# Performance work log

Hardware: AMD Instinct MI355X
Metric: run time of the kernel (lower is better)

The kernel has to match this reference:

```python
import jax, jax.numpy as jnp
import numpy as np

B, L, M, H = 16, 1024, 1024, 128
NEG = -1e30


def setup_inputs() -> dict:
    key = jax.random.key(0)
    ks = jax.random.split(key, 8)
    return {
        "text": jax.random.normal(ks[0], (B, L, H), dtype=jnp.float32),
        "modality": jax.random.normal(ks[1], (B, M, H), dtype=jnp.float32),
        "text_mask": jax.random.randint(ks[2], (B, L), 0, 2, dtype=jnp.int32),
        "modality_mask": jax.random.randint(ks[3], (B, M), 0, 2, dtype=jnp.int32),
        # learned parameters (xavier-uniform style scale)
        "text_weight": jax.random.normal(ks[4], (H, 1), dtype=jnp.float32) * 0.1,
        "modality_weight": jax.random.normal(ks[5], (H, 1), dtype=jnp.float32) * 0.1,
        "text_modality_weight": jax.random.normal(ks[6], (1, 1, H), dtype=jnp.float32) * 0.1,
        "bias": jnp.zeros((1,), dtype=jnp.float32),
    }


def reference(text, modality, text_mask, modality_mask,
              text_weight, modality_weight, text_modality_weight, bias):
    # similarity matrix s: (B, L, M)   (eval mode: dropout is identity)
    s0 = jnp.matmul(text, text_weight)                      # (B, L, 1)
    s1 = jnp.swapaxes(jnp.matmul(modality, modality_weight), 1, 2)  # (B, 1, M)
    s2 = jnp.einsum('blh,bmh->blm', text * text_modality_weight, modality)
    s = s0 + s1 + s2 + bias                                 # (B, L, M)

    mmask = modality_mask[:, None, :].astype(jnp.float32)   # (B, 1, M)
    tmask = text_mask[:, :, None].astype(jnp.float32)       # (B, L, 1)
    p1 = jax.nn.softmax(mmask * s + (1.0 - mmask) * NEG, axis=2)  # text->modality
    p2 = jax.nn.softmax(tmask * s + (1.0 - tmask) * NEG, axis=1)  # modality->text

    a = jnp.matmul(p1, modality)                            # (B, L, H)
    b = jnp.matmul(jnp.matmul(p1, jnp.swapaxes(p2, 1, 2)), text)  # (B, L, H)
    return jnp.concatenate([text, a, text * a, text * b], axis=2)  # (B, L, 8H)
```

## Files before the change

kernel.cpp:

```cpp
#include <hip/hip_runtime.h>

#define B_ 16
#define L_ 1024
#define M_ 1024
#define H_ 128

typedef unsigned short u16;
typedef unsigned int u32;
typedef __bf16 bf16x8 __attribute__((ext_vector_type(8)));
typedef float f32x4 __attribute__((ext_vector_type(4)));

__device__ __forceinline__ u16 f2bf(float x){
  u32 u = __float_as_uint(x);
  u = (u + 0x7fffu + ((u >> 16) & 1u)) >> 16;
  return (u16)u;
}

__global__ __launch_bounds__(256) void zero_f32(float4* __restrict__ p, int n4)
{
  int i = blockIdx.x * 256 + threadIdx.x;
  int stride = gridDim.x * 256;
  for (; i < n4; i += stride) p[i] = make_float4(0.f, 0.f, 0.f, 0.f);
}

__global__ __launch_bounds__(256) void prep2(
    const float* __restrict__ text, const float* __restrict__ modality,
    const int* __restrict__ tmask, const int* __restrict__ mmask,
    const float* __restrict__ tw, const float* __restrict__ mw,
    const float* __restrict__ tmw,
    u16* __restrict__ textw_bf, u16* __restrict__ mod_bf,
    u16* __restrict__ textT_bf, u16* __restrict__ modT_bf,
    float* __restrict__ t0, float* __restrict__ s1m)
{
  int g = blockIdx.x;
  int sel = g >> 8;
  int b = (g >> 4) & 15;
  int r0 = (g & 15) * 64;
  const float* src = (sel ? modality : text) + ((size_t)b * 1024 + r0) * H_;
  const int* msk = (sel ? mmask : tmask) + b * 1024 + r0;
  const float* dotw = sel ? mw : tw;
  u16* rowout = (sel ? mod_bf : textw_bf) + ((size_t)b * 1024 + r0) * H_;
  u16* trout = (sel ? modT_bf : textT_bf) + (size_t)b * H_ * 1024 + r0;
  float* dotout = (sel ? s1m : t0) + b * 1024 + r0;

  __shared__ u16 tile[128][72];
  int tid = threadIdx.x;
  int rgrp = tid >> 5;
  int lane32 = tid & 31;
  int h0 = lane32 * 4;
  float4 w4 = *(const float4*)&dotw[h0];
  float4 mv = sel ? make_float4(1.f, 1.f, 1.f, 1.f) : *(const float4*)&tmw[h0];
  float dpart[8];
  #pragma unroll
  for (int p = 0; p < 8; p++) {
    int row = rgrp + p * 8;
    float4 x = *(const float4*)&src[(size_t)row * H_ + h0];
    dpart[p] = x.x * w4.x + x.y * w4.y + x.z * w4.z + x.w * w4.w;
    uint2 pk;
    pk.x = (u32)f2bf(x.x * mv.x) | ((u32)f2bf(x.y * mv.y) << 16);
    pk.y = (u32)f2bf(x.z * mv.z) | ((u32)f2bf(x.w * mv.w) << 16);
    *(uint2*)&rowout[(size_t)row * H_ + h0] = pk;
    int mk = msk[row];
    tile[h0 + 0][row] = mk ? f2bf(x.x) : (u16)0;
    tile[h0 + 1][row] = mk ? f2bf(x.y) : (u16)0;
    tile[h0 + 2][row] = mk ? f2bf(x.z) : (u16)0;
    tile[h0 + 3][row] = mk ? f2bf(x.w) : (u16)0;
  }
  #pragma unroll
  for (int p = 0; p < 8; p++) {
    float d = dpart[p];
    #pragma unroll
    for (int off = 1; off < 32; off <<= 1) d += __shfl_xor(d, off);
    if (lane32 == 0) dotout[rgrp + p * 8] = d;
  }
  __syncthreads();
  int lcol = (tid & 7) * 8;
  #pragma unroll
  for (int p = 0; p < 4; p++) {
    int h = (tid >> 3) + p * 32;
    uint4 v = *(const uint4*)&tile[h][lcol];
    *(uint4*)&trout[(size_t)h * 1024 + lcol] = v;
  }
}

__global__ __launch_bounds__(256) void gemm_exp(
    const u16* __restrict__ A, const u16* __restrict__ Bm,
    const float* __restrict__ t0, const float* __restrict__ s1m,
    const float* __restrict__ bias, const int* __restrict__ tmask,
    const int* __restrict__ mmask, float* __restrict__ rowsum,
    float* __restrict__ colsum, u16* __restrict__ ET)
{
  int f = blockIdx.x;
  int orig = (f & 7) * 256 + (f >> 3);
  int b = orig >> 7;
  int a0 = (orig & 15) * 64, b0 = ((orig >> 4) & 7) * 128;
  int tid = threadIdx.x, lane = tid & 63, wid = tid >> 6;
  int wr = wid >> 1, wc = wid & 1;
  int c = lane & 15, q = lane >> 4;
  __shared__ __align__(16) char smem[24576];
  const u16* Ab = A + (size_t)(b * L_ + a0) * H_;
  const u16* Bb = Bm + (size_t)(b * M_ + b0) * H_;
  f32x4 acc[2][4];
  #pragma unroll
  for (int i = 0; i < 2; i++)
    #pragma unroll
    for (int j = 0; j < 4; j++) acc[i][j] = (f32x4){0.f, 0.f, 0.f, 0.f};
  for (int kt = 0; kt < 2; kt++) {
    __syncthreads();
    #pragma unroll
    for (int i = 0; i < 2; i++) {
      int cc = tid + 256 * i;
      int row = cc >> 3, col8 = cc & 7;
      uint4 v = *(const uint4*)(Ab + (size_t)row * H_ + kt * 64 + col8 * 8);
      *(uint4*)(smem + row * 128 + ((col8 * 16) ^ ((row & 7) << 4))) = v;
    }
    #pragma unroll
    for (int i = 0; i < 4; i++) {
      int cc = tid + 256 * i;
      int row = cc >> 3, col8 = cc & 7;
      uint4 v = *(const uint4*)(Bb + (size_t)row * H_ + kt * 64 + col8 * 8);
      *(uint4*)(smem + 8192 + row * 128 + ((col8 * 16) ^ ((row & 7) << 4))) = v;
    }
    __syncthreads();
    #pragma unroll
    for (int kk = 0; kk < 2; kk++) {
      int kbyte = kk * 64 + (q << 4);
      bf16x8 af[2], bfr[4];
      #pragma unroll
      for (int i = 0; i < 2; i++) {
        int ra = wr * 32 + i * 16 + c;
        af[i] = *(const bf16x8*)(smem + ra * 128 + (kbyte ^ ((ra & 7) << 4)));
      }
      #pragma unroll
      for (int j = 0; j < 4; j++) {
        int rb = wc * 64 + j * 16 + c;
        bfr[j] = *(const bf16x8*)(smem + 8192 + rb * 128 + (kbyte ^ ((rb & 7) << 4)));
      }
      #pragma unroll
      for (int i = 0; i < 2; i++)
        #pragma unroll
        for (int j = 0; j < 4; j++)
          acc[i][j] = __builtin_amdgcn_mfma_f32_16x16x32_bf16(af[i], bfr[j], acc[i][j], 0, 0, 0);
    }
  }
  float biasv = bias[0];
  float t0v[2][4];
  int tmv[2][4];
  #pragma unroll
  for (int i = 0; i < 2; i++)
    #pragma unroll
    for (int r = 0; r < 4; r++) {
      int ar = a0 + wr * 32 + i * 16 + q * 4 + r;
      t0v[i][r] = t0[b * L_ + ar];
      tmv[i][r] = tmask[b * L_ + ar];
    }
  float s1v[4];
  int mmv[4];
  #pragma unroll
  for (int j = 0; j < 4; j++) {
    int gcol = b0 + wc * 64 + j * 16 + c;
    s1v[j] = s1m[b * M_ + gcol];
    mmv[j] = mmask[b * M_ + gcol];
  }
  float ev[2][4][4];
  #pragma unroll
  for (int i = 0; i < 2; i++)
    #pragma unroll
    for (int j = 0; j < 4; j++)
      #pragma unroll
      for (int r = 0; r < 4; r++)
        ev[i][j][r] = __expf(acc[i][j][r] + t0v[i][r] + s1v[j] + biasv);
  #pragma unroll
  for (int i = 0; i < 2; i++)
    #pragma unroll
    for (int r = 0; r < 4; r++) {
      float prs = 0.f;
      #pragma unroll
      for (int j = 0; j < 4; j++) prs += mmv[j] ? ev[i][j][r] : 0.f;
      #pragma unroll
      for (int off = 1; off < 16; off <<= 1) prs += __shfl_xor(prs, off);
      if (c == 0) {
        int ar = a0 + wr * 32 + i * 16 + q * 4 + r;
        atomicAdd(&rowsum[b * L_ + ar], prs);
      }
    }
  #pragma unroll
  for (int j = 0; j < 4; j++) {
    float pcs = 0.f;
    #pragma unroll
    for (int i = 0; i < 2; i++)
      #pragma unroll
      for (int r = 0; r < 4; r++) pcs += tmv[i][r] ? ev[i][j][r] : 0.f;
    pcs += __shfl_xor(pcs, 16);
    pcs += __shfl_xor(pcs, 32);
    if (q == 0) {
      int gcol = b0 + wc * 64 + j * 16 + c;
      atomicAdd(&colsum[b * M_ + gcol], pcs);
    }
  }
  __syncthreads();
  u16* et = (u16*)smem;
  #pragma unroll
  for (int i = 0; i < 2; i++)
    #pragma unroll
    for (int j = 0; j < 4; j++) {
      int gcolL = wc * 64 + j * 16 + c;
      int arL = wr * 32 + i * 16 + q * 4;
      u32 lo = (u32)f2bf(ev[i][j][0]) | ((u32)f2bf(ev[i][j][1]) << 16);
      u32 hi = (u32)f2bf(ev[i][j][2]) | ((u32)f2bf(ev[i][j][3]) << 16);
      uint2 pk; pk.x = lo; pk.y = hi;
      *(uint2*)&et[gcolL * 72 + arL] = pk;
    }
  __syncthreads();
  #pragma unroll
  for (int it = 0; it < 4; it++) {
    int mrow = (tid >> 3) + it * 32;
    int l8 = tid & 7;
    uint4 v = *(const uint4*)&et[mrow * 72 + l8 * 8];
    *(uint4*)&ET[((size_t)(b * M_ + b0 + mrow)) * L_ + a0 + l8 * 8] = v;
  }
}

__global__ __launch_bounds__(512) void gemm_ct(
    const u16* __restrict__ A, const u16* __restrict__ ET,
    float* __restrict__ c_f32)
{
  int f = blockIdx.x;
  int orig = (f & 7) * 64 + (f >> 3);
  int b = orig >> 5;
  int x = orig & 3, y = (orig >> 2) & 7;
  int ia = x & 1, ks = x >> 1;
  int a0 = ia * 64, b0 = y * 128;
  int tid = threadIdx.x, lane = tid & 63, wid = tid >> 6;
  int wr = wid >> 2, wc = wid & 3;
  int c = lane & 15, q = lane >> 4;
  __shared__ __align__(16) char smem[24576];
  const u16* Ab = A + (size_t)(b * H_ + a0) * L_;
  const u16* Bb = ET + (size_t)(b * M_ + b0) * L_;
  f32x4 acc[2][2];
  #pragma unroll
  for (int i = 0; i < 2; i++)
    #pragma unroll
    for (int j = 0; j < 2; j++) acc[i][j] = (f32x4){0.f, 0.f, 0.f, 0.f};
  for (int kt = ks * 8; kt < ks * 8 + 8; kt++) {
    __syncthreads();
    {
      int row = tid >> 3, col8 = tid & 7;
      uint4 v = *(const uint4*)(Ab + (size_t)row * L_ + kt * 64 + col8 * 8);
      *(uint4*)(smem + row * 128 + ((col8 * 16) ^ ((row & 7) << 4))) = v;
    }
    #pragma unroll
    for (int i = 0; i < 2; i++) {
      int cc = tid + 512 * i;
      int row = cc >> 3, col8 = cc & 7;
      uint4 v = *(const uint4*)(Bb + (size_t)row * L_ + kt * 64 + col8 * 8);
      *(uint4*)(smem + 8192 + row * 128 + ((col8 * 16) ^ ((row & 7) << 4))) = v;
    }
    __syncthreads();
    #pragma unroll
    for (int kk = 0; kk < 2; kk++) {
      int kbyte = kk * 64 + (q << 4);
      bf16x8 af[2], bfr[2];
      #pragma unroll
      for (int i = 0; i < 2; i++) {
        int ra = wr * 32 + i * 16 + c;
        af[i] = *(const bf16x8*)(smem + ra * 128 + (kbyte ^ ((ra & 7) << 4)));
      }
      #pragma unroll
      for (int j = 0; j < 2; j++) {
        int rb = wc * 32 + j * 16 + c;
        bfr[j] = *(const bf16x8*)(smem + 8192 + rb * 128 + (kbyte ^ ((rb & 7) << 4)));
      }
      #pragma unroll
      for (int i = 0; i < 2; i++)
        #pragma unroll
        for (int j = 0; j < 2; j++)
          acc[i][j] = __builtin_amdgcn_mfma_f32_16x16x32_bf16(af[i], bfr[j], acc[i][j], 0, 0, 0);
    }
  }
  #pragma unroll
  for (int i = 0; i < 2; i++)
    #pragma unroll
    for (int j = 0; j < 2; j++) {
      int arow0 = a0 + wr * 32 + i * 16 + q * 4;
      int gcol = b0 + wc * 32 + j * 16 + c;
      #pragma unroll
      for (int r = 0; r < 4; r++)
        atomicAdd(&c_f32[((size_t)(b * H_ + arow0 + r)) * M_ + gcol], acc[i][j][r]);
    }
}

__global__ __launch_bounds__(512) void gemm_ab(
    const u16* __restrict__ ET, const u16* __restrict__ B1,
    const float* __restrict__ c_f32, const float* __restrict__ colsum,
    const int* __restrict__ mmask, const float* __restrict__ rowsum,
    const float* __restrict__ text, float* __restrict__ out)
{
  int f = blockIdx.x;
  int orig = (f & 7) * 32 + (f >> 3);
  int b = orig >> 4;
  int a0 = (orig & 15) * 64;
  int tid = threadIdx.x, lane = tid & 63, wid = tid >> 6;
  int wr = wid >> 2, wc = wid & 3;
  int c = lane & 15, q = lane >> 4;
  __shared__ __align__(16) u16 At[64 * 76];
  __shared__ __align__(16) char Bs[2][16384];
  __shared__ float invcm[1024];
  const u16* ETb = ET + (size_t)b * M_ * L_;
  const u16* B1b = B1 + (size_t)b * H_ * M_;
  const float* cfb = c_f32 + (size_t)b * H_ * M_;
  for (int i = tid; i < 1024; i += 512)
    invcm[i] = mmask[b * M_ + i] ? 1.0f / fmaxf(colsum[b * M_ + i], 1e-30f) : 0.f;
  f32x4 acc_a[2][2], acc_b[2][2];
  #pragma unroll
  for (int i = 0; i < 2; i++)
    #pragma unroll
    for (int j = 0; j < 2; j++) {
      acc_a[i][j] = (f32x4){0.f, 0.f, 0.f, 0.f};
      acc_b[i][j] = (f32x4){0.f, 0.f, 0.f, 0.f};
    }
  for (int kt = 0; kt < 16; kt++) {
    __syncthreads();
    {
      int mloc = tid >> 3, l8 = tid & 7;
      uint4 v = *(const uint4*)&ETb[((size_t)(kt * 64 + mloc)) * L_ + a0 + l8 * 8];
      u16* rp = At + mloc * 76 + l8 * 8;
      uint2 p0; p0.x = v.x; p0.y = v.y;
      uint2 p1; p1.x = v.z; p1.y = v.w;
      *(uint2*)rp = p0;
      *(uint2*)(rp + 4) = p1;
    }
    #pragma unroll
    for (int i = 0; i < 2; i++) {
      int cc = tid + 512 * i;
      int row = cc >> 3, col8 = cc & 7;
      uint4 v1 = *(const uint4*)(B1b + (size_t)row * M_ + kt * 64 + col8 * 8);
      *(uint4*)(Bs[0] + row * 128 + ((col8 * 16) ^ ((row & 7) << 4))) = v1;
      int mbase = kt * 64 + col8 * 8;
      float4 xa = *(const float4*)&cfb[(size_t)row * M_ + mbase];
      float4 xb = *(const float4*)&cfb[(size_t)row * M_ + mbase + 4];
      float4 ia4 = *(const float4*)&invcm[mbase];
      float4 ib4 = *(const float4*)&invcm[mbase + 4];
      uint4 v2;
      v2.x = (u32)f2bf(xa.x * ia4.x) | ((u32)f2bf(xa.y * ia4.y) << 16);
      v2.y = (u32)f2bf(xa.z * ia4.z) | ((u32)f2bf(xa.w * ia4.w) << 16);
      v2.z = (u32)f2bf(xb.x * ib4.x) | ((u32)f2bf(xb.y * ib4.y) << 16);
      v2.w = (u32)f2bf(xb.z * ib4.z) | ((u32)f2bf(xb.w * ib4.w) << 16);
      *(uint4*)(Bs[1] + row * 128 + ((col8 * 16) ^ ((row & 7) << 4))) = v2;
    }
    __syncthreads();
    #pragma unroll
    for (int kk = 0; kk < 2; kk++) {
      int kbyte = kk * 64 + (q << 4);
      bf16x8 af[2], b1f[2], b2f[2];
      #pragma unroll
      for (int i = 0; i < 2; i++) {
        int lidx = wr * 32 + i * 16 + c;
        int mbase = kk * 32 + q * 8;
        union { unsigned short s[8]; bf16x8 v; } ua;
        #pragma unroll
        for (int e = 0; e < 8; e++) ua.s[e] = At[(mbase + e) * 76 + lidx];
        af[i] = ua.v;
      }
      #pragma unroll
      for (int j = 0; j < 2; j++) {
        int rb = wc * 32 + j * 16 + c;
        b1f[j] = *(const bf16x8*)(Bs[0] + rb * 128 + (kbyte ^ ((rb & 7) << 4)));
        b2f[j] = *(const bf16x8*)(Bs[1] + rb * 128 + (kbyte ^ ((rb & 7) << 4)));
      }
      #pragma unroll
      for (int i = 0; i < 2; i++)
        #pragma unroll
        for (int j = 0; j < 2; j++) {
          acc_a[i][j] = __builtin_amdgcn_mfma_f32_16x16x32_bf16(af[i], b1f[j], acc_a[i][j], 0, 0, 0);
          acc_b[i][j] = __builtin_amdgcn_mfma_f32_16x16x32_bf16(af[i], b2f[j], acc_b[i][j], 0, 0, 0);
        }
    }
  }
  float irs[2][4];
  #pragma unroll
  for (int i = 0; i < 2; i++)
    #pragma unroll
    for (int r = 0; r < 4; r++) {
      int ar = a0 + wr * 32 + i * 16 + q * 4 + r;
      irs[i][r] = 1.0f / fmaxf(rowsum[b * L_ + ar], 1e-30f);
    }
  #pragma unroll
  for (int i = 0; i < 2; i++)
    #pragma unroll
    for (int j = 0; j < 2; j++) {
      int gcol = wc * 32 + j * 16 + c;
      #pragma unroll
      for (int r = 0; r < 4; r++) {
        int ar = a0 + wr * 32 + i * 16 + q * 4 + r;
        float av = acc_a[i][j][r] * irs[i][r];
        float bv = acc_b[i][j][r] * irs[i][r];
        float tv = text[((size_t)(b * L_ + ar)) * H_ + gcol];
        size_t base = ((size_t)(b * L_ + ar)) * 512 + gcol;
        out[base] = tv;
        out[base + 128] = av;
        out[base + 256] = tv * av;
        out[base + 384] = tv * bv;
      }
    }
}

extern "C" void kernel_launch(void* const* d_in, const int* in_sizes, int n_in,
                              void* d_out, int out_size, void* d_ws, size_t ws_size,
                              hipStream_t stream) {
  const float* text = (const float*)d_in[0];
  const float* modality = (const float*)d_in[1];
  const int* text_mask = (const int*)d_in[2];
  const int* modality_mask = (const int*)d_in[3];
  const float* text_weight = (const float*)d_in[4];
  const float* modality_weight = (const float*)d_in[5];
  const float* tmw = (const float*)d_in[6];
  const float* bias = (const float*)d_in[7];
  float* out = (float*)d_out;
  (void)in_sizes; (void)n_in; (void)out_size; (void)ws_size;

  char* ws = (char*)d_ws;
  size_t off = 0;
  auto alloc = [&](size_t bytes) { void* p = ws + off; off += (bytes + 255) & ~(size_t)255; return p; };
  u16*   ET       = (u16*)  alloc((size_t)B_ * M_ * L_ * 2);
  u16*   textw_bf = (u16*)  alloc((size_t)B_ * L_ * H_ * 2);
  u16*   mod_bf   = (u16*)  alloc((size_t)B_ * M_ * H_ * 2);
  u16*   textT_bf = (u16*)  alloc((size_t)B_ * H_ * L_ * 2);
  u16*   mod_bfT  = (u16*)  alloc((size_t)B_ * H_ * M_ * 2);
  float* t0       = (float*)alloc((size_t)B_ * L_ * 4);
  float* s1m      = (float*)alloc((size_t)B_ * M_ * 4);
  float* rowsum   = (float*)alloc((size_t)B_ * L_ * 4);
  float* colsum   = (float*)alloc((size_t)B_ * M_ * 4);
  float* c_f32    = (float*)alloc((size_t)B_ * H_ * M_ * 4);

  int n4 = (B_ * (L_ + M_) + B_ * H_ * M_) / 4;
  zero_f32<<<2048, 256, 0, stream>>>((float4*)rowsum, n4);
  prep2<<<512, 256, 0, stream>>>(text, modality, text_mask, modality_mask,
      text_weight, modality_weight, tmw,
      textw_bf, mod_bf, textT_bf, mod_bfT, t0, s1m);
  gemm_exp<<<2048, 256, 0, stream>>>(textw_bf, mod_bf, t0, s1m, bias,
      text_mask, modality_mask, rowsum, colsum, ET);
  gemm_ct<<<512, 512, 0, stream>>>(textT_bf, ET, c_f32);
  gemm_ab<<<256, 512, 0, stream>>>(ET, mod_bfT, c_f32, colsum, modality_mask,
      rowsum, text, out);
}
```

Before: 181.2 us.

## Double the gemm_ab block to 1024 threads and prefetch next K tile into registers

gemm_ab now runs with 1024 threads (16 waves), each wave owning a 32x16 output tile instead of 32x32. It also stages global loads for the next K tile into registers while MFMAs run on the current shared-memory tile. Both aim to hide global memory latency in a grid of only 256 blocks that cannot fill the GPU. The cost is more register pressure per thread under the larger launch bound, an extra barrier per iteration, and less MFMA work per wave.

```diff
diff --git a/kernel.cpp b/kernel.cpp
--- a/kernel.cpp
+++ b/kernel.cpp
@@ -290,7 +290,7 @@
     }
 }
 
-__global__ __launch_bounds__(512) void gemm_ab(
+__global__ __launch_bounds__(1024) void gemm_ab(
     const u16* __restrict__ ET, const u16* __restrict__ B1,
     const float* __restrict__ c_f32, const float* __restrict__ colsum,
     const int* __restrict__ mmask, const float* __restrict__ rowsum,
@@ -301,7 +301,7 @@
   int b = orig >> 4;
   int a0 = (orig & 15) * 64;
   int tid = threadIdx.x, lane = tid & 63, wid = tid >> 6;
-  int wr = wid >> 2, wc = wid & 3;
+  int wr = wid >> 3, wc = wid & 7;
   int c = lane & 15, q = lane >> 4;
   __shared__ __align__(16) u16 At[64 * 76];
   __shared__ __align__(16) char Bs[2][16384];
@@ -309,50 +309,53 @@
   const u16* ETb = ET + (size_t)b * M_ * L_;
   const u16* B1b = B1 + (size_t)b * H_ * M_;
   const float* cfb = c_f32 + (size_t)b * H_ * M_;
-  for (int i = tid; i < 1024; i += 512)
-    invcm[i] = mmask[b * M_ + i] ? 1.0f / fmaxf(colsum[b * M_ + i], 1e-30f) : 0.f;
-  f32x4 acc_a[2][2], acc_b[2][2];
-  #pragma unroll
-  for (int i = 0; i < 2; i++)
-    #pragma unroll
-    for (int j = 0; j < 2; j++) {
-      acc_a[i][j] = (f32x4){0.f, 0.f, 0.f, 0.f};
-      acc_b[i][j] = (f32x4){0.f, 0.f, 0.f, 0.f};
-    }
+  invcm[tid] = mmask[b * M_ + tid] ? 1.0f / fmaxf(colsum[b * M_ + tid], 1e-30f) : 0.f;
+
+  int sArow = tid >> 4, sAcol = (tid & 15) * 4;
+  int sBrow = tid >> 3, sBcol8 = tid & 7;
+
+  f32x4 acc_a[2], acc_b[2];
+  #pragma unroll
+  for (int i = 0; i < 2; i++) {
+    acc_a[i] = (f32x4){0.f, 0.f, 0.f, 0.f};
+    acc_b[i] = (f32x4){0.f, 0.f, 0.f, 0.f};
+  }
+
+  uint2 rA;
+  uint4 rB1;
+  float4 rB2a, rB2b;
+  auto LOAD = [&](int kt) {
+    rA = *(const uint2*)&ETb[((size_t)(kt * 64 + sArow)) * L_ + a0 + sAcol];
+    int mbase = kt * 64 + sBcol8 * 8;
+    rB1 = *(const uint4*)(B1b + (size_t)sBrow * M_ + mbase);
+    rB2a = *(const float4*)&cfb[(size_t)sBrow * M_ + mbase];
+    rB2b = *(const float4*)&cfb[(size_t)sBrow * M_ + mbase + 4];
+  };
+  auto WRITE = [&](int kt) {
+    *(uint2*)(At + sArow * 76 + sAcol) = rA;
+    int swz = (sBcol8 * 16) ^ ((sBrow & 7) << 4);
+    *(uint4*)(Bs[0] + sBrow * 128 + swz) = rB1;
+    int mbase = kt * 64 + sBcol8 * 8;
+    float4 ia4 = *(const float4*)&invcm[mbase];
+    float4 ib4 = *(const float4*)&invcm[mbase + 4];
+    uint4 v2;
+    v2.x = (u32)f2bf(rB2a.x * ia4.x) | ((u32)f2bf(rB2a.y * ia4.y) << 16);
+    v2.y = (u32)f2bf(rB2a.z * ia4.z) | ((u32)f2bf(rB2a.w * ia4.w) << 16);
+    v2.z = (u32)f2bf(rB2b.x * ib4.x) | ((u32)f2bf(rB2b.y * ib4.y) << 16);
+    v2.w = (u32)f2bf(rB2b.z * ib4.z) | ((u32)f2bf(rB2b.w * ib4.w) << 16);
+    *(uint4*)(Bs[1] + sBrow * 128 + swz) = v2;
+  };
+
+  LOAD(0);
+  __syncthreads();
+  WRITE(0);
   for (int kt = 0; kt < 16; kt++) {
-    __syncthreads();
-    {
-      int mloc = tid >> 3, l8 = tid & 7;
-      uint4 v = *(const uint4*)&ETb[((size_t)(kt * 64 + mloc)) * L_ + a0 + l8 * 8];
-      u16* rp = At + mloc * 76 + l8 * 8;
-      uint2 p0; p0.x = v.x; p0.y = v.y;
-      uint2 p1; p1.x = v.z; p1.y = v.w;
-      *(uint2*)rp = p0;
-      *(uint2*)(rp + 4) = p1;
-    }
-    #pragma unroll
-    for (int i = 0; i < 2; i++) {
-      int cc = tid + 512 * i;
-      int row = cc >> 3, col8 = cc & 7;
-      uint4 v1 = *(const uint4*)(B1b + (size_t)row * M_ + kt * 64 + col8 * 8);
-      *(uint4*)(Bs[0] + row * 128 + ((col8 * 16) ^ ((row & 7) << 4))) = v1;
-      int mbase = kt * 64 + col8 * 8;
-      float4 xa = *(const float4*)&cfb[(size_t)row * M_ + mbase];
-      float4 xb = *(const float4*)&cfb[(size_t)row * M_ + mbase + 4];
-      float4 ia4 = *(const float4*)&invcm[mbase];
-      float4 ib4 = *(const float4*)&invcm[mbase + 4];
-      uint4 v2;
-      v2.x = (u32)f2bf(xa.x * ia4.x) | ((u32)f2bf(xa.y * ia4.y) << 16);
-      v2.y = (u32)f2bf(xa.z * ia4.z) | ((u32)f2bf(xa.w * ia4.w) << 16);
-      v2.z = (u32)f2bf(xb.x * ib4.x) | ((u32)f2bf(xb.y * ib4.y) << 16);
-      v2.w = (u32)f2bf(xb.z * ib4.z) | ((u32)f2bf(xb.w * ib4.w) << 16);
-      *(uint4*)(Bs[1] + row * 128 + ((col8 * 16) ^ ((row & 7) << 4))) = v2;
-    }
+    if (kt < 15) LOAD(kt + 1);
     __syncthreads();
     #pragma unroll
     for (int kk = 0; kk < 2; kk++) {
       int kbyte = kk * 64 + (q << 4);
-      bf16x8 af[2], b1f[2], b2f[2];
+      bf16x8 af[2], b1f, b2f;
       #pragma unroll
       for (int i = 0; i < 2; i++) {
         int lidx = wr * 32 + i * 16 + c;
@@ -362,21 +365,19 @@
         for (int e = 0; e < 8; e++) ua.s[e] = At[(mbase + e) * 76 + lidx];
         af[i] = ua.v;
       }
-      #pragma unroll
-      for (int j = 0; j < 2; j++) {
-        int rb = wc * 32 + j * 16 + c;
-        b1f[j] = *(const bf16x8*)(Bs[0] + rb * 128 + (kbyte ^ ((rb & 7) << 4)));
-        b2f[j] = *(const bf16x8*)(Bs[1] + rb * 128 + (kbyte ^ ((rb & 7) << 4)));
-      }
-      #pragma unroll
-      for (int i = 0; i < 2; i++)
-        #pragma unroll
-        for (int j = 0; j < 2; j++) {
-          acc_a[i][j] = __builtin_amdgcn_mfma_f32_16x16x32_bf16(af[i], b1f[j], acc_a[i][j], 0, 0, 0);
-          acc_b[i][j] = __builtin_amdgcn_mfma_f32_16x16x32_bf16(af[i], b2f[j], acc_b[i][j], 0, 0, 0);
-        }
-    }
-  }
+      int rb = wc * 16 + c;
+      b1f = *(const bf16x8*)(Bs[0] + rb * 128 + (kbyte ^ ((rb & 7) << 4)));
+      b2f = *(const bf16x8*)(Bs[1] + rb * 128 + (kbyte ^ ((rb & 7) << 4)));
+      #pragma unroll
+      for (int i = 0; i < 2; i++) {
+        acc_a[i] = __builtin_amdgcn_mfma_f32_16x16x32_bf16(af[i], b1f, acc_a[i], 0, 0, 0);
+        acc_b[i] = __builtin_amdgcn_mfma_f32_16x16x32_bf16(af[i], b2f, acc_b[i], 0, 0, 0);
+      }
+    }
+    __syncthreads();
+    if (kt < 15) WRITE(kt + 1);
+  }
+
   float irs[2][4];
   #pragma unroll
   for (int i = 0; i < 2; i++)
@@ -385,24 +386,22 @@
       int ar = a0 + wr * 32 + i * 16 + q * 4 + r;
       irs[i][r] = 1.0f / fmaxf(rowsum[b * L_ + ar], 1e-30f);
     }
-  #pragma unroll
-  for (int i = 0; i < 2; i++)
-    #pragma unroll
-    for (int j = 0; j < 2; j++) {
-      int gcol = wc * 32 + j * 16 + c;
-      #pragma unroll
-      for (int r = 0; r < 4; r++) {
-        int ar = a0 + wr * 32 + i * 16 + q * 4 + r;
-        float av = acc_a[i][j][r] * irs[i][r];
-        float bv = acc_b[i][j][r] * irs[i][r];
-        float tv = text[((size_t)(b * L_ + ar)) * H_ + gcol];
-        size_t base = ((size_t)(b * L_ + ar)) * 512 + gcol;
-        out[base] = tv;
-        out[base + 128] = av;
-        out[base + 256] = tv * av;
-        out[base + 384] = tv * bv;
-      }
-    }
+  int gcol = wc * 16 + c;
+  #pragma unroll
+  for (int i = 0; i < 2; i++) {
+    #pragma unroll
+    for (int r = 0; r < 4; r++) {
+      int ar = a0 + wr * 32 + i * 16 + q * 4 + r;
+      float av = acc_a[i][r] * irs[i][r];
+      float bv = acc_b[i][r] * irs[i][r];
+      float tv = text[((size_t)(b * L_ + ar)) * H_ + gcol];
+      size_t base = ((size_t)(b * L_ + ar)) * 512 + gcol;
+      out[base] = tv;
+      out[base + 128] = av;
+      out[base + 256] = tv * av;
+      out[base + 384] = tv * bv;
+    }
+  }
 }
 
 extern "C" void kernel_launch(void* const* d_in, const int* in_sizes, int n_in,
@@ -441,6 +440,6 @@
   gemm_exp<<<2048, 256, 0, stream>>>(textw_bf, mod_bf, t0, s1m, bias,
       text_mask, modality_mask, rowsum, colsum, ET);
   gemm_ct<<<512, 512, 0, stream>>>(textT_bf, ET, c_f32);
-  gemm_ab<<<256, 512, 0, stream>>>(ET, mod_bfT, c_f32, colsum, modality_mask,
+  gemm_ab<<<256, 1024, 0, stream>>>(ET, mod_bfT, c_f32, colsum, modality_mask,
       rowsum, text, out);
 }
```

Result: faster. 166.0 us (-8.4%).
